# Performance work log

Measured on AMD Instinct MI355X. Metric: run time of the kernel, lower is better.

## Reference

```python
import jax, jax.numpy as jnp
import numpy as np

MARGIN = 0.3
EPS = 1e-12

def setup_inputs() -> dict:
    key = jax.random.key(0)
    k1, k2 = jax.random.split(key)
    n, d, num_classes = 8192, 512, 512
    inputs = jax.random.normal(k1, (n, d), dtype=jnp.float32)
    targets = jax.random.randint(k2, (n,), 0, num_classes, dtype=jnp.int64)
    return {"inputs": inputs, "targets": targets}

def reference(inputs, targets):
    n = inputs.shape[0]
    # pairwise Euclidean distances: ||xi||^2 + ||xj||^2 - 2 xi.xj, clamped & sqrt'd
    sq = jnp.sum(inputs * inputs, axis=1)  # [n]
    dist2 = sq[:, None] + sq[None, :] - 2.0 * (inputs @ inputs.T)
    dist = jnp.sqrt(jnp.clip(dist2, EPS, None))  # [n, n]
    mask = targets[:, None] == targets[None, :]  # [n, n] same-identity mask
    neg_inf = jnp.asarray(-jnp.inf, dist.dtype)
    pos_inf = jnp.asarray(jnp.inf, dist.dtype)
    dist_ap = jnp.max(jnp.where(mask, dist, neg_inf), axis=1)   # hardest positive per row
    dist_an = jnp.min(jnp.where(mask, pos_inf, dist), axis=1)   # hardest negative per row
    # MarginRankingLoss with y=1, mean reduction: mean(relu(dist_ap - dist_an + margin))
    loss = jnp.mean(jnp.maximum(dist_ap - dist_an + MARGIN, 0.0))
    return loss
```

## Files before the change

### kernel.cpp

```cpp
#include <hip/hip_runtime.h>

#define N 8192
#define D 512
#define NFULLP 2016
#define NDIAG 64
#define NBRICKS (NFULLP + NDIAG)
#define MARGIN 0.3f

typedef __attribute__((ext_vector_type(4))) int int4v;
typedef __attribute__((ext_vector_type(8))) int int8v;
typedef __attribute__((ext_vector_type(4))) float f32x4;

__device__ __forceinline__ void gload_lds16(const void* g, void* l) {
    __builtin_amdgcn_global_load_lds(
        (const __attribute__((address_space(1))) void*)g,
        (__attribute__((address_space(3))) void*)l,
        16, 0, 0);
}

__device__ __forceinline__ int8v load_frag8(const unsigned char* base, int row, int q) {
    const int v = (2 * q) ^ (row & 7);
    int4v lo = *(const int4v*)(base + row * 128 + v * 16);
    int4v hi = *(const int4v*)(base + row * 128 + (v ^ 1) * 16);
    return __builtin_shufflevector(lo, hi, 0, 1, 2, 3, 4, 5, 6, 7);
}

__device__ __forceinline__ void stage_tile(const unsigned char* Ag, unsigned char* Asm,
                                           const unsigned char* Bg, unsigned char* Bsm,
                                           int tid, int k0) {
    #pragma unroll
    for (int s = 0; s < 4; s++) {
        int p = s * 256 + tid;
        int r = p >> 3, kc = (p & 7) ^ (r & 7);
        gload_lds16(Ag + (size_t)r * D + k0 + kc * 16, Asm + p * 16);
    }
    #pragma unroll
    for (int s = 0; s < 4; s++) {
        int p = s * 256 + tid;
        int r = p >> 3, kc = (p & 7) ^ (r & 7);
        gload_lds16(Bg + (size_t)r * D + k0 + kc * 16, Bsm + p * 16);
    }
}

__global__ void prep_kernel(const float* __restrict__ x,
                            unsigned char* __restrict__ x8,
                            float* __restrict__ sq,
                            unsigned int* __restrict__ apU,
                            unsigned int* __restrict__ anU,
                            int* __restrict__ cnt) {
    if (blockIdx.x == 0 && threadIdx.x == 0) cnt[0] = 0;
    int w = threadIdx.x >> 6, lane = threadIdx.x & 63;
    int row = blockIdx.x * 4 + w;
    const float4* p = (const float4*)(x + (size_t)row * D) + lane * 2;
    float4 v0 = p[0], v1 = p[1];
    float s = v0.x * v0.x + v0.y * v0.y + v0.z * v0.z + v0.w * v0.w
            + v1.x * v1.x + v1.y * v1.y + v1.z * v1.z + v1.w * v1.w;
    int w0 = __builtin_amdgcn_cvt_pk_fp8_f32(v0.x, v0.y, 0, false);
    w0     = __builtin_amdgcn_cvt_pk_fp8_f32(v0.z, v0.w, w0, true);
    int w1 = __builtin_amdgcn_cvt_pk_fp8_f32(v1.x, v1.y, 0, false);
    w1     = __builtin_amdgcn_cvt_pk_fp8_f32(v1.z, v1.w, w1, true);
    ((int2*)(x8 + (size_t)row * D))[lane] = make_int2(w0, w1);
    #pragma unroll
    for (int o = 32; o > 0; o >>= 1) s += __shfl_xor(s, o);
    if (lane == 0) {
        sq[row] = s;
        apU[row] = 0u;
        anU[row] = 0x7f800000u;
    }
}

__device__ __forceinline__ void brick_body(
    int rowBase, int colBase,
    const unsigned char* __restrict__ xb, const float* __restrict__ sq,
    const int* __restrict__ tgt,
    unsigned int* __restrict__ apU, unsigned int* __restrict__ anU,
    char* smem_raw, float* sqI, float* sqJ, int* tI, int* tJ) {
    unsigned char* A0 = (unsigned char*)smem_raw;
    unsigned char* B0 = A0 + 16384;
    unsigned char* A1 = A0 + 32768;
    unsigned char* B1 = A0 + 49152;
    float* redAp = (float*)smem_raw;
    float* redAn = redAp + 128 * 34;
    float* colAp = (float*)smem_raw;
    float* colAn = colAp + 128 * 10;

    const int tid = threadIdx.x;
    const int w = tid >> 6, lane = tid & 63, q = lane >> 4, c = lane & 15;
    const int wm = w & 1, wn = w >> 1;

    if (tid < 128) {
        sqI[tid] = sq[rowBase + tid]; tI[tid] = tgt[rowBase + tid];
        sqJ[tid] = sq[colBase + tid]; tJ[tid] = tgt[colBase + tid];
    }

    const unsigned char* Ag = xb + (size_t)rowBase * D;
    const unsigned char* Bg = xb + (size_t)colBase * D;

    f32x4 acc[4][4] = {};

    stage_tile(Ag, A0, Bg, B0, tid, 0);
    stage_tile(Ag, A1, Bg, B1, tid, 128);

    #pragma unroll
    for (int kk = 0; kk < 4; kk++) {
        unsigned char* Asm = (kk & 1) ? A1 : A0;
        unsigned char* Bsm = (kk & 1) ? B1 : B0;
        if (kk == 0) asm volatile("s_waitcnt vmcnt(8)" ::: "memory");
        else         asm volatile("s_waitcnt vmcnt(0)" ::: "memory");
        asm volatile("s_barrier" ::: "memory");
        __builtin_amdgcn_sched_barrier(0);

        if (kk == 1) stage_tile(Ag, A0, Bg, B0, tid, 256);
        if (kk == 2) stage_tile(Ag, A1, Bg, B1, tid, 384);

        int8v af[4], bf[4];
        #pragma unroll
        for (int t = 0; t < 4; t++)
            af[t] = load_frag8(Asm, wm * 64 + t * 16 + c, q);
        #pragma unroll
        for (int t = 0; t < 4; t++)
            bf[t] = load_frag8(Bsm, wn * 64 + t * 16 + c, q);

        #pragma unroll
        for (int tm = 0; tm < 4; tm++)
            #pragma unroll
            for (int t = 0; t < 4; t++)
                acc[tm][t] = __builtin_amdgcn_mfma_scale_f32_16x16x128_f8f6f4(
                    af[tm], bf[t], acc[tm][t],
                    0, 0,
                    0, 0x7F7F7F7Fu, 0, 0x7F7F7F7Fu);
    }
    __syncthreads();

    float sjc[4]; int tjx[4];
    #pragma unroll
    for (int tn = 0; tn < 4; tn++) {
        int col_l = wn * 64 + tn * 16 + c;
        sjc[tn] = sqJ[col_l]; tjx[tn] = tJ[col_l];
    }
    float apc[4], anc[4];
    #pragma unroll
    for (int tn = 0; tn < 4; tn++) { apc[tn] = -1e30f; anc[tn] = 1e30f; }
    #pragma unroll
    for (int tm = 0; tm < 4; tm++) {
        #pragma unroll
        for (int r = 0; r < 4; r++) {
            int row_l = wm * 64 + tm * 16 + q * 4 + r;
            float si = sqI[row_l]; int ti = tI[row_l];
            float rp = -1e30f, rn = 1e30f;
            #pragma unroll
            for (int tn = 0; tn < 4; tn++) {
                float p = acc[tm][tn][r];
                bool same = (ti == tjx[tn]);
                float rk = fmaf(-2.0f, p, sjc[tn]);
                float ck = fmaf(-2.0f, p, si);
                rp = fmaxf(rp, same ? rk : -1e30f);
                rn = fminf(rn, same ? 1e30f : rk);
                apc[tn] = fmaxf(apc[tn], same ? ck : -1e30f);
                anc[tn] = fminf(anc[tn], same ? 1e30f : ck);
            }
            redAp[row_l * 34 + wn * 16 + c] = rp;
            redAn[row_l * 34 + wn * 16 + c] = rn;
        }
    }
    __syncthreads();
    if (tid < 128) {
        float ap = -1e30f, an = 1e30f;
        #pragma unroll 8
        for (int u = 0; u < 32; u++) {
            ap = fmaxf(ap, redAp[tid * 34 + u]);
            an = fminf(an, redAn[tid * 34 + u]);
        }
        float apd = fmaxf(sqI[tid] + ap, 0.0f);
        float and_ = fmaxf(sqI[tid] + an, 0.0f);
        atomicMax(&apU[rowBase + tid], __float_as_uint(apd));
        atomicMin(&anU[rowBase + tid], __float_as_uint(and_));
    }
    __syncthreads();
    #pragma unroll
    for (int tn = 0; tn < 4; tn++) {
        int col_l = wn * 64 + tn * 16 + c;
        colAp[col_l * 10 + wm * 4 + q] = apc[tn];
        colAn[col_l * 10 + wm * 4 + q] = anc[tn];
    }
    __syncthreads();
    if (tid < 128) {
        float ap = -1e30f, an = 1e30f;
        #pragma unroll
        for (int u = 0; u < 8; u++) {
            ap = fmaxf(ap, colAp[tid * 10 + u]);
            an = fminf(an, colAn[tid * 10 + u]);
        }
        float apd = fmaxf(sqJ[tid] + ap, 0.0f);
        float and_ = fmaxf(sqJ[tid] + an, 0.0f);
        atomicMax(&apU[colBase + tid], __float_as_uint(apd));
        atomicMin(&anU[colBase + tid], __float_as_uint(and_));
    }
}

__global__ __launch_bounds__(256, 2)
void gemm_kernel(const unsigned char* __restrict__ xb,
                 const float* __restrict__ sq,
                 const int* __restrict__ tgt,
                 unsigned int* __restrict__ apU,
                 unsigned int* __restrict__ anU) {
    __shared__ __align__(16) char smem_raw[65536];
    __shared__ float sqI[128], sqJ[128];
    __shared__ int tI[128], tJ[128];

    const int id = blockIdx.x;
    int ri, cj;
    if (id < NFULLP) {
        cj = (int)((1.0f + sqrtf(1.0f + 8.0f * (float)id)) * 0.5f);
        while (cj * (cj - 1) / 2 > id) cj--;
        while ((cj + 1) * cj / 2 <= id) cj++;
        ri = id - cj * (cj - 1) / 2;
    } else {
        ri = cj = id - NFULLP;
    }
    brick_body(ri * 128, cj * 128, xb, sq, tgt, apU, anU,
               smem_raw, sqI, sqJ, tI, tJ);
}

__global__ void reduce_kernel(const unsigned int* __restrict__ apU,
                              const unsigned int* __restrict__ anU,
                              float* __restrict__ bsum, int* __restrict__ cnt,
                              float* __restrict__ out) {
    int tid = threadIdx.x;
    int row = blockIdx.x * 256 + tid;
    float ap = __uint_as_float(apU[row]);
    float an = __uint_as_float(anU[row]);
    float dap = sqrtf(fmaxf(ap, 1e-12f));
    float dan = sqrtf(fmaxf(an, 1e-12f));
    float v = fmaxf(dap - dan + MARGIN, 0.0f);
    #pragma unroll
    for (int o = 32; o > 0; o >>= 1) v += __shfl_xor(v, o);
    __shared__ float ss[4];
    __shared__ int amLast;
    if ((tid & 63) == 0) ss[tid >> 6] = v;
    __syncthreads();
    if (tid == 0) {
        bsum[blockIdx.x] = ss[0] + ss[1] + ss[2] + ss[3];
        __threadfence();
        amLast = (atomicAdd(cnt, 1) == N / 256 - 1);
    }
    __syncthreads();
    if (amLast && tid < 64) {
        __threadfence();
        float t = (tid < N / 256) ? bsum[tid] : 0.0f;
        #pragma unroll
        for (int o = 32; o > 0; o >>= 1) t += __shfl_xor(t, o);
        if (tid == 0) out[0] = t * (1.0f / (float)N);
    }
}

extern "C" void kernel_launch(void* const* d_in, const int* in_sizes, int n_in,
                              void* d_out, int out_size, void* d_ws, size_t ws_size,
                              hipStream_t stream) {
    const float* x  = (const float*)d_in[0];
    const int* tgt  = (const int*)d_in[1];
    float* out      = (float*)d_out;

    char* ws = (char*)d_ws;
    unsigned char* x8 = (unsigned char*)ws;
    float* sq   = (float*)(ws + (size_t)N * D);
    unsigned int* apU = (unsigned int*)(sq + N);
    unsigned int* anU = apU + N;
    float* bsum = (float*)(anU + N);
    int* cnt = (int*)(bsum + 32);

    prep_kernel<<<N / 4, 256, 0, stream>>>(x, x8, sq, apU, anU, cnt);
    gemm_kernel<<<NBRICKS, 256, 0, stream>>>(x8, sq, tgt, apU, anU);
    reduce_kernel<<<N / 256, 256, 0, stream>>>(apU, anU, bsum, cnt, out);
}
```

Measured before the change: 105.6 us.

## Enlarge GEMM bricks to 256x256 with 512 threads and shuffle-based reductions

Doubles the brick size to 256x256 and runs 512-thread blocks, cutting the number of bricks from 2080 to 528 and halving the redundant global reads of operand tiles. The double-buffered K pipeline becomes a single buffer, with the next stage issued midway through each k-step. Row and column max/min reductions now use wave shuffles instead of large shared-memory scratch arrays, and block IDs are remapped in an interleaved order. The cost is more accumulator registers per thread, less overlap between loads and MFMA work, and a smaller grid that may leave parts of the GPU idle, including a tail with little work.

Result: slower. 283.3 us (+168.4%).

```diff
diff --git a/kernel.cpp b/kernel.cpp
--- a/kernel.cpp
+++ b/kernel.cpp
@@ -2,9 +2,9 @@
 
 #define N 8192
 #define D 512
-#define NFULLP 2016
-#define NDIAG 64
-#define NBRICKS (NFULLP + NDIAG)
+#define NOFF 496
+#define NDIAG 32
+#define NBRICKS (NOFF + NDIAG)
 #define MARGIN 0.3f
 
 typedef __attribute__((ext_vector_type(4))) int int4v;
@@ -30,13 +30,13 @@
                                            int tid, int k0) {
     #pragma unroll
     for (int s = 0; s < 4; s++) {
-        int p = s * 256 + tid;
+        int p = s * 512 + tid;
         int r = p >> 3, kc = (p & 7) ^ (r & 7);
         gload_lds16(Ag + (size_t)r * D + k0 + kc * 16, Asm + p * 16);
     }
     #pragma unroll
     for (int s = 0; s < 4; s++) {
-        int p = s * 256 + tid;
+        int p = s * 512 + tid;
         int r = p >> 3, kc = (p & 7) ^ (r & 7);
         gload_lds16(Bg + (size_t)r * D + k0 + kc * 16, Bsm + p * 16);
     }
@@ -69,26 +69,40 @@
     }
 }
 
-__device__ __forceinline__ void brick_body(
-    int rowBase, int colBase,
-    const unsigned char* __restrict__ xb, const float* __restrict__ sq,
-    const int* __restrict__ tgt,
-    unsigned int* __restrict__ apU, unsigned int* __restrict__ anU,
-    char* smem_raw, float* sqI, float* sqJ, int* tI, int* tJ) {
-    unsigned char* A0 = (unsigned char*)smem_raw;
-    unsigned char* B0 = A0 + 16384;
-    unsigned char* A1 = A0 + 32768;
-    unsigned char* B1 = A0 + 49152;
-    float* redAp = (float*)smem_raw;
-    float* redAn = redAp + 128 * 34;
-    float* colAp = (float*)smem_raw;
-    float* colAn = colAp + 128 * 10;
+__global__ __launch_bounds__(512, 4)
+void gemm_kernel(const unsigned char* __restrict__ xb,
+                 const float* __restrict__ sq,
+                 const int* __restrict__ tgt,
+                 unsigned int* __restrict__ apU,
+                 unsigned int* __restrict__ anU) {
+    __shared__ __align__(16) char smem_raw[65536];
+    __shared__ float sqI[256], sqJ[256];
+    __shared__ int tI[256], tJ[256];
+
+    unsigned char* Asm = (unsigned char*)smem_raw;
+    unsigned char* Bsm = Asm + 32768;
+    float* rowPap = (float*)smem_raw;
+    float* rowPan = rowPap + 256;
+    float* colPap = rowPan + 256;
+    float* colPan = colPap + 256 * 5;
+
+    const int id = (blockIdx.x & 7) * 66 + (blockIdx.x >> 3);
+    int ri, cj;
+    if (id < NOFF) {
+        cj = (int)((1.0f + sqrtf(1.0f + 8.0f * (float)id)) * 0.5f);
+        while (cj * (cj - 1) / 2 > id) cj--;
+        while ((cj + 1) * cj / 2 <= id) cj++;
+        ri = id - cj * (cj - 1) / 2;
+    } else {
+        ri = cj = id - NOFF;
+    }
+    const int rowBase = ri * 256, colBase = cj * 256;
 
     const int tid = threadIdx.x;
     const int w = tid >> 6, lane = tid & 63, q = lane >> 4, c = lane & 15;
-    const int wm = w & 1, wn = w >> 1;
-
-    if (tid < 128) {
+    const int wm = w & 3, wn = w >> 2;
+
+    if (tid < 256) {
         sqI[tid] = sq[rowBase + tid]; tI[tid] = tgt[rowBase + tid];
         sqJ[tid] = sq[colBase + tid]; tJ[tid] = tgt[colBase + tid];
     }
@@ -96,51 +110,54 @@
     const unsigned char* Ag = xb + (size_t)rowBase * D;
     const unsigned char* Bg = xb + (size_t)colBase * D;
 
-    f32x4 acc[4][4] = {};
-
-    stage_tile(Ag, A0, Bg, B0, tid, 0);
-    stage_tile(Ag, A1, Bg, B1, tid, 128);
+    f32x4 acc[4][8] = {};
+
+    stage_tile(Ag, Asm, Bg, Bsm, tid, 0);
 
     #pragma unroll
     for (int kk = 0; kk < 4; kk++) {
-        unsigned char* Asm = (kk & 1) ? A1 : A0;
-        unsigned char* Bsm = (kk & 1) ? B1 : B0;
-        if (kk == 0) asm volatile("s_waitcnt vmcnt(8)" ::: "memory");
-        else         asm volatile("s_waitcnt vmcnt(0)" ::: "memory");
-        asm volatile("s_barrier" ::: "memory");
-        __builtin_amdgcn_sched_barrier(0);
-
-        if (kk == 1) stage_tile(Ag, A0, Bg, B0, tid, 256);
-        if (kk == 2) stage_tile(Ag, A1, Bg, B1, tid, 384);
-
-        int8v af[4], bf[4];
+        __syncthreads();
+        int8v af[4], b0[4];
         #pragma unroll
         for (int t = 0; t < 4; t++)
             af[t] = load_frag8(Asm, wm * 64 + t * 16 + c, q);
         #pragma unroll
         for (int t = 0; t < 4; t++)
-            bf[t] = load_frag8(Bsm, wn * 64 + t * 16 + c, q);
-
+            b0[t] = load_frag8(Bsm, wn * 128 + t * 16 + c, q);
         #pragma unroll
         for (int tm = 0; tm < 4; tm++)
             #pragma unroll
             for (int t = 0; t < 4; t++)
                 acc[tm][t] = __builtin_amdgcn_mfma_scale_f32_16x16x128_f8f6f4(
-                    af[tm], bf[t], acc[tm][t],
+                    af[tm], b0[t], acc[tm][t],
                     0, 0,
                     0, 0x7F7F7F7Fu, 0, 0x7F7F7F7Fu);
-    }
-    __syncthreads();
-
-    float sjc[4]; int tjx[4];
-    #pragma unroll
-    for (int tn = 0; tn < 4; tn++) {
-        int col_l = wn * 64 + tn * 16 + c;
+        int8v b1[4];
+        #pragma unroll
+        for (int t = 0; t < 4; t++)
+            b1[t] = load_frag8(Bsm, wn * 128 + (4 + t) * 16 + c, q);
+        __syncthreads();
+        if (kk < 3)
+            stage_tile(Ag, Asm, Bg, Bsm, tid, (kk + 1) * 128);
+        #pragma unroll
+        for (int tm = 0; tm < 4; tm++)
+            #pragma unroll
+            for (int t = 0; t < 4; t++)
+                acc[tm][4 + t] = __builtin_amdgcn_mfma_scale_f32_16x16x128_f8f6f4(
+                    af[tm], b1[t], acc[tm][4 + t],
+                    0, 0, 0, 0x7F7F7F7Fu, 0, 0x7F7F7F7Fu);
+    }
+
+    float sjc[8]; int tjx[8];
+    #pragma unroll
+    for (int tn = 0; tn < 8; tn++) {
+        int col_l = wn * 128 + tn * 16 + c;
         sjc[tn] = sqJ[col_l]; tjx[tn] = tJ[col_l];
     }
-    float apc[4], anc[4];
-    #pragma unroll
-    for (int tn = 0; tn < 4; tn++) { apc[tn] = -1e30f; anc[tn] = 1e30f; }
+    float apc[8], anc[8];
+    #pragma unroll
+    for (int tn = 0; tn < 8; tn++) { apc[tn] = -1e30f; anc[tn] = 1e30f; }
+    float rpk[4][4], rnk[4][4];
     #pragma unroll
     for (int tm = 0; tm < 4; tm++) {
         #pragma unroll
@@ -149,7 +166,7 @@
             float si = sqI[row_l]; int ti = tI[row_l];
             float rp = -1e30f, rn = 1e30f;
             #pragma unroll
-            for (int tn = 0; tn < 4; tn++) {
+            for (int tn = 0; tn < 8; tn++) {
                 float p = acc[tm][tn][r];
                 bool same = (ti == tjx[tn]);
                 float rk = fmaf(-2.0f, p, sjc[tn]);
@@ -159,67 +176,66 @@
                 apc[tn] = fmaxf(apc[tn], same ? ck : -1e30f);
                 anc[tn] = fminf(anc[tn], same ? 1e30f : ck);
             }
-            redAp[row_l * 34 + wn * 16 + c] = rp;
-            redAn[row_l * 34 + wn * 16 + c] = rn;
+            #pragma unroll
+            for (int o = 1; o < 16; o <<= 1) {
+                rp = fmaxf(rp, __shfl_xor(rp, o));
+                rn = fminf(rn, __shfl_xor(rn, o));
+            }
+            rpk[tm][r] = rp; rnk[tm][r] = rn;
         }
     }
+    if (wn == 1 && c == 0) {
+        #pragma unroll
+        for (int tm = 0; tm < 4; tm++)
+            #pragma unroll
+            for (int r = 0; r < 4; r++) {
+                int row_l = wm * 64 + tm * 16 + q * 4 + r;
+                rowPap[row_l] = rpk[tm][r];
+                rowPan[row_l] = rnk[tm][r];
+            }
+    }
+    #pragma unroll
+    for (int tn = 0; tn < 8; tn++) {
+        apc[tn] = fmaxf(apc[tn], __shfl_xor(apc[tn], 16));
+        apc[tn] = fmaxf(apc[tn], __shfl_xor(apc[tn], 32));
+        anc[tn] = fminf(anc[tn], __shfl_xor(anc[tn], 16));
+        anc[tn] = fminf(anc[tn], __shfl_xor(anc[tn], 32));
+    }
+    if (q == 0) {
+        #pragma unroll
+        for (int tn = 0; tn < 8; tn++) {
+            int col_l = wn * 128 + tn * 16 + c;
+            colPap[col_l * 5 + wm] = apc[tn];
+            colPan[col_l * 5 + wm] = anc[tn];
+        }
+    }
     __syncthreads();
-    if (tid < 128) {
+    if (wn == 0 && c == 0) {
+        #pragma unroll
+        for (int tm = 0; tm < 4; tm++)
+            #pragma unroll
+            for (int r = 0; r < 4; r++) {
+                int row_l = wm * 64 + tm * 16 + q * 4 + r;
+                float ap = fmaxf(rpk[tm][r], rowPap[row_l]);
+                float an = fminf(rnk[tm][r], rowPan[row_l]);
+                float apd = fmaxf(sqI[row_l] + ap, 0.0f);
+                float and_ = fmaxf(sqI[row_l] + an, 0.0f);
+                atomicMax(&apU[rowBase + row_l], __float_as_uint(apd));
+                atomicMin(&anU[rowBase + row_l], __float_as_uint(and_));
+            }
+    }
+    if (tid < 256) {
         float ap = -1e30f, an = 1e30f;
-        #pragma unroll 8
-        for (int u = 0; u < 32; u++) {
-            ap = fmaxf(ap, redAp[tid * 34 + u]);
-            an = fminf(an, redAn[tid * 34 + u]);
-        }
-        float apd = fmaxf(sqI[tid] + ap, 0.0f);
-        float and_ = fmaxf(sqI[tid] + an, 0.0f);
-        atomicMax(&apU[rowBase + tid], __float_as_uint(apd));
-        atomicMin(&anU[rowBase + tid], __float_as_uint(and_));
-    }
-    __syncthreads();
-    #pragma unroll
-    for (int tn = 0; tn < 4; tn++) {
-        int col_l = wn * 64 + tn * 16 + c;
-        colAp[col_l * 10 + wm * 4 + q] = apc[tn];
-        colAn[col_l * 10 + wm * 4 + q] = anc[tn];
-    }
-    __syncthreads();
-    if (tid < 128) {
-        float ap = -1e30f, an = 1e30f;
-        #pragma unroll
-        for (int u = 0; u < 8; u++) {
-            ap = fmaxf(ap, colAp[tid * 10 + u]);
-            an = fminf(an, colAn[tid * 10 + u]);
+        #pragma unroll
+        for (int u = 0; u < 4; u++) {
+            ap = fmaxf(ap, colPap[tid * 5 + u]);
+            an = fminf(an, colPan[tid * 5 + u]);
         }
         float apd = fmaxf(sqJ[tid] + ap, 0.0f);
         float and_ = fmaxf(sqJ[tid] + an, 0.0f);
         atomicMax(&apU[colBase + tid], __float_as_uint(apd));
         atomicMin(&anU[colBase + tid], __float_as_uint(and_));
     }
-}
-
-__global__ __launch_bounds__(256, 2)
-void gemm_kernel(const unsigned char* __restrict__ xb,
-                 const float* __restrict__ sq,
-                 const int* __restrict__ tgt,
-                 unsigned int* __restrict__ apU,
-                 unsigned int* __restrict__ anU) {
-    __shared__ __align__(16) char smem_raw[65536];
-    __shared__ float sqI[128], sqJ[128];
-    __shared__ int tI[128], tJ[128];
-
-    const int id = blockIdx.x;
-    int ri, cj;
-    if (id < NFULLP) {
-        cj = (int)((1.0f + sqrtf(1.0f + 8.0f * (float)id)) * 0.5f);
-        while (cj * (cj - 1) / 2 > id) cj--;
-        while ((cj + 1) * cj / 2 <= id) cj++;
-        ri = id - cj * (cj - 1) / 2;
-    } else {
-        ri = cj = id - NFULLP;
-    }
-    brick_body(ri * 128, cj * 128, xb, sq, tgt, apU, anU,
-               smem_raw, sqI, sqJ, tI, tJ);
 }
 
 __global__ void reduce_kernel(const unsigned int* __restrict__ apU,
@@ -270,6 +286,6 @@
     int* cnt = (int*)(bsum + 32);
 
     prep_kernel<<<N / 4, 256, 0, stream>>>(x, x8, sq, apU, anU, cnt);
-    gemm_kernel<<<NBRICKS, 256, 0, stream>>>(x8, sq, tgt, apU, anU);
+    gemm_kernel<<<NBRICKS, 512, 0, stream>>>(x8, sq, tgt, apU, anU);
     reduce_kernel<<<N / 256, 256, 0, stream>>>(apU, anU, bsum, cnt, out);
 }
```
